# Optimization experiments

Hardware: AMD Instinct MI355X
Metric: run time of the kernel (lower is better)

The kernel has to match this reference:

```python
import jax, jax.numpy as jnp
import numpy as np

N_NODES = 50000
N_EDGES = 800000
IN_CH = 256
HID = 256
NUM_GRAPHS = 512
LEAKY_SLOPE = 0.01
EPS = 1e-5


def gcn_conv(x, src, dst, W, b):
    # src/dst already include self loops. Symmetric normalization D^-1/2 A_hat D^-1/2.
    deg = jnp.zeros((N_NODES,), x.dtype).at[dst].add(1.0)
    dinv = jax.lax.rsqrt(deg)  # deg >= 1 because of self loops
    norm = dinv[src] * dinv[dst]  # [E+N]
    h = x @ W  # [N, H] dense GEMM
    agg = jnp.zeros((N_NODES, W.shape[1]), x.dtype).at[dst].add(h[src] * norm[:, None])
    return agg + b


def layer_norm(x, w, b):
    mu = jnp.mean(x, axis=-1, keepdims=True)
    var = jnp.mean(jnp.square(x - mu), axis=-1, keepdims=True)
    return (x - mu) * jax.lax.rsqrt(var + EPS) * w + b


def setup_inputs() -> dict:
    key = jax.random.key(0)
    ks = jax.random.split(key, 8)
    x = jax.random.normal(ks[0], (N_NODES, IN_CH), dtype=jnp.float32)
    edge_index = jax.random.randint(ks[1], (2, N_EDGES), 0, N_NODES, dtype=jnp.int64)
    batch = jnp.sort(jax.random.randint(ks[2], (N_NODES,), 0, NUM_GRAPHS, dtype=jnp.int64))
    s1 = (2.0 / IN_CH) ** 0.5
    s2 = (2.0 / HID) ** 0.5
    W1 = jax.random.normal(ks[3], (IN_CH, HID), dtype=jnp.float32) * s1
    b1 = jnp.zeros((HID,), jnp.float32)
    W2 = jax.random.normal(ks[4], (HID, HID), dtype=jnp.float32) * s2
    b2 = jnp.zeros((HID,), jnp.float32)
    ln1_w = jnp.ones((HID,), jnp.float32)
    ln1_b = jnp.zeros((HID,), jnp.float32)
    ln2_w = jnp.ones((HID,), jnp.float32)
    ln2_b = jnp.zeros((HID,), jnp.float32)
    return {"x": x, "edge_index": edge_index, "batch": batch,
            "W1": W1, "b1": b1, "ln1_w": ln1_w, "ln1_b": ln1_b,
            "W2": W2, "b2": b2, "ln2_w": ln2_w, "ln2_b": ln2_b}


def reference(x, edge_index, batch, W1, b1, ln1_w, ln1_b, W2, b2, ln2_w, ln2_b):
    loop = jnp.arange(N_NODES, dtype=edge_index.dtype)
    src = jnp.concatenate([edge_index[0], loop])
    dst = jnp.concatenate([edge_index[1], loop])

    h = gcn_conv(x, src, dst, W1, b1)
    h = layer_norm(h, ln1_w, ln1_b)
    h = jnp.where(h >= 0, h, LEAKY_SLOPE * h)

    h = gcn_conv(h, src, dst, W2, b2)
    h = layer_norm(h, ln2_w, ln2_b)
    h = jnp.where(h >= 0, h, LEAKY_SLOPE * h)

    # global mean pool per graph (dropout is inference no-op)
    sums = jax.ops.segment_sum(h, batch, num_segments=NUM_GRAPHS)
    cnts = jax.ops.segment_sum(jnp.ones((N_NODES,), h.dtype), batch, num_segments=NUM_GRAPHS)
    return sums / jnp.maximum(cnts, 1.0)[:, None]
```

## Files before the change

### kernel.cpp

```cpp
#include <hip/hip_runtime.h>

#define N_NODES 50000
#define N_EDGES 800000
#define CH 256
#define NUM_GRAPHS 512
#define LEAKY 0.01f
#define LN_EPS 1e-5f
#define NBLK ((N_NODES + 255) / 256)

typedef __attribute__((ext_vector_type(4))) float f32x4;
typedef __attribute__((ext_vector_type(2))) float f32x2;
typedef __attribute__((ext_vector_type(8))) short bf16x8;

__device__ __forceinline__ float b2f(unsigned short u) {
    union { unsigned int i; float f; } x; x.i = ((unsigned int)u) << 16; return x.f;
}
__device__ __forceinline__ unsigned short f2b(float f) {
    union { float f; unsigned int i; } x; x.f = f;
    unsigned int r = x.i + 0x7fffu + ((x.i >> 16) & 1u);
    return (unsigned short)(r >> 16);
}
__device__ __forceinline__ f32x2 b2f2(unsigned int u) {
    union { unsigned int i; float f; } lo, hi;
    lo.i = u << 16; hi.i = u & 0xffff0000u;
    f32x2 r; r.x = lo.f; r.y = hi.f; return r;
}
__device__ __forceinline__ unsigned int pack2(float a, float b) {
    return (unsigned int)f2b(a) | ((unsigned int)f2b(b) << 16);
}

__global__ void zero_ints(int* __restrict__ p, int n) {
    int i = blockIdx.x * blockDim.x + threadIdx.x;
    if (i < n) p[i] = 0;
}

__global__ void count_deg(const int* __restrict__ dst, int* __restrict__ cnt) {
    int e = blockIdx.x * blockDim.x + threadIdx.x;
    if (e < N_EDGES) atomicAdd(&cnt[dst[e]], 1);
}

__global__ __launch_bounds__(256) void block_reduce(const int* __restrict__ cnt,
                                                    int* __restrict__ bsum,
                                                    float* __restrict__ dinv) {
    __shared__ int s[256];
    int tid = threadIdx.x;
    int i = blockIdx.x * 256 + tid;
    int v = (i < N_NODES) ? cnt[i] : 0;
    if (i < N_NODES) dinv[i] = rsqrtf(1.0f + (float)v);
    s[tid] = v;
    __syncthreads();
    #pragma unroll
    for (int off = 128; off > 0; off >>= 1) {
        if (tid < off) s[tid] += s[tid + off];
        __syncthreads();
    }
    if (tid == 0) bsum[blockIdx.x] = s[0];
}

__global__ __launch_bounds__(256) void scan_bsums(int* __restrict__ bsum) {
    __shared__ int s[256];
    int tid = threadIdx.x;
    int v = (tid < NBLK) ? bsum[tid] : 0;
    s[tid] = v;
    __syncthreads();
    #pragma unroll
    for (int off = 1; off < 256; off <<= 1) {
        int t = (tid >= off) ? s[tid - off] : 0;
        __syncthreads();
        s[tid] += t;
        __syncthreads();
    }
    if (tid < NBLK) bsum[tid] = s[tid] - v;
}

__global__ __launch_bounds__(256) void block_scan(const int* __restrict__ cnt,
                                                  const int* __restrict__ bsum,
                                                  int* __restrict__ rowptr,
                                                  int* __restrict__ cursor) {
    __shared__ int s[256];
    int tid = threadIdx.x;
    int i = blockIdx.x * 256 + tid;
    int v = (i < N_NODES) ? cnt[i] : 0;
    s[tid] = v;
    __syncthreads();
    #pragma unroll
    for (int off = 1; off < 256; off <<= 1) {
        int t = (tid >= off) ? s[tid - off] : 0;
        __syncthreads();
        s[tid] += t;
        __syncthreads();
    }
    if (i < N_NODES) {
        int val = bsum[blockIdx.x] + s[tid] - v;
        rowptr[i] = val;
        cursor[i] = val;
        if (i == N_NODES - 1) rowptr[N_NODES] = bsum[blockIdx.x] + s[tid];
    }
}

__global__ void fill_csr(const int* __restrict__ src, const int* __restrict__ dst,
                         int* __restrict__ cursor, int* __restrict__ col) {
    int e = blockIdx.x * blockDim.x + threadIdx.x;
    if (e < N_EDGES) {
        int d = dst[e];
        int p = atomicAdd(&cursor[d], 1);
        col[p] = src[e];
    }
}

__global__ void transpose_w(const float* __restrict__ W, unsigned short* __restrict__ WT) {
    int k = blockIdx.x;
    int n = threadIdx.x;
    WT[n * CH + k] = f2b(W[k * CH + n]);
}

#define BM 128
#define BN 128
#define BK 64
#define SWZ(row, kb) (((row) * 128 + (kb) * 16) ^ (((row) & 7) << 4))

__global__ __launch_bounds__(256) void gemm_bf16(const unsigned short* __restrict__ A,
                                                 const unsigned short* __restrict__ BT,
                                                 const float* __restrict__ dinv,
                                                 unsigned short* __restrict__ out) {
    __shared__ unsigned short As[BM * BK];
    __shared__ unsigned short Bs[BN * BK];
    const int row0 = blockIdx.x * BM;
    const int col0 = blockIdx.y * BN;
    const int tid = threadIdx.x;
    const int w = tid >> 6, l = tid & 63;
    const int wr = w >> 1, wc = w & 1;
    const int lr = l & 15, lg = l >> 4;

    f32x4 acc[4][4] = {};

    for (int k0 = 0; k0 < CH; k0 += BK) {
        #pragma unroll
        for (int it = 0; it < 4; it++) {
            int cidx = it * 256 + tid;
            int r = cidx >> 3, kb = cidx & 7;
            int grow = row0 + r;
            uint4 va = make_uint4(0u, 0u, 0u, 0u);
            if (grow < N_NODES) va = *(const uint4*)&A[(size_t)grow * CH + k0 + kb * 8];
            *(uint4*)((char*)As + SWZ(r, kb)) = va;
            uint4 vb = *(const uint4*)&BT[(size_t)(col0 + r) * CH + k0 + kb * 8];
            *(uint4*)((char*)Bs + SWZ(r, kb)) = vb;
        }
        __syncthreads();
        #pragma unroll
        for (int ks = 0; ks < 2; ks++) {
            bf16x8 af[4], bfr[4];
            #pragma unroll
            for (int fm = 0; fm < 4; fm++) {
                int r = wr * 64 + fm * 16 + lr;
                af[fm] = *(const bf16x8*)((const char*)As + SWZ(r, ks * 4 + lg));
            }
            #pragma unroll
            for (int fn = 0; fn < 4; fn++) {
                int r = wc * 64 + fn * 16 + lr;
                bfr[fn] = *(const bf16x8*)((const char*)Bs + SWZ(r, ks * 4 + lg));
            }
            #pragma unroll
            for (int fm = 0; fm < 4; fm++)
                #pragma unroll
                for (int fn = 0; fn < 4; fn++)
                    acc[fm][fn] = __builtin_amdgcn_mfma_f32_16x16x32_bf16(af[fm], bfr[fn], acc[fm][fn], 0, 0, 0);
        }
        __syncthreads();
    }
    #pragma unroll
    for (int fm = 0; fm < 4; fm++) {
        #pragma unroll
        for (int r = 0; r < 4; r++) {
            int grow = row0 + wr * 64 + fm * 16 + lg * 4 + r;
            if (grow < N_NODES) {
                float s = dinv[grow];
                #pragma unroll
                for (int fn = 0; fn < 4; fn++) {
                    int gcol = col0 + wc * 64 + fn * 16 + lr;
                    out[(size_t)grow * CH + gcol] = f2b(acc[fm][fn][r] * s);
                }
            }
        }
    }
}

__global__ __launch_bounds__(256) void gemm_f32a(const float* __restrict__ Af,
                                                 const unsigned short* __restrict__ BT,
                                                 const float* __restrict__ dinv,
                                                 unsigned short* __restrict__ out) {
    __shared__ unsigned short As[BM * BK];
    __shared__ unsigned short Bs[BN * BK];
    const int row0 = blockIdx.x * BM;
    const int col0 = blockIdx.y * BN;
    const int tid = threadIdx.x;
    const int w = tid >> 6, l = tid & 63;
    const int wr = w >> 1, wc = w & 1;
    const int lr = l & 15, lg = l >> 4;

    f32x4 acc[4][4] = {};

    for (int k0 = 0; k0 < CH; k0 += BK) {
        #pragma unroll
        for (int it = 0; it < 4; it++) {
            int cidx = it * 256 + tid;
            int r = cidx >> 3, kb = cidx & 7;
            int grow = row0 + r;
            uint4 ua = make_uint4(0u, 0u, 0u, 0u);
            if (grow < N_NODES) {
                const float* ap = &Af[(size_t)grow * CH + k0 + kb * 8];
                float4 v0 = *(const float4*)ap;
                float4 v1 = *(const float4*)(ap + 4);
                ua = make_uint4(pack2(v0.x, v0.y), pack2(v0.z, v0.w),
                                pack2(v1.x, v1.y), pack2(v1.z, v1.w));
            }
            *(uint4*)((char*)As + SWZ(r, kb)) = ua;
            uint4 vb = *(const uint4*)&BT[(size_t)(col0 + r) * CH + k0 + kb * 8];
            *(uint4*)((char*)Bs + SWZ(r, kb)) = vb;
        }
        __syncthreads();
        #pragma unroll
        for (int ks = 0; ks < 2; ks++) {
            bf16x8 af[4], bfr[4];
            #pragma unroll
            for (int fm = 0; fm < 4; fm++) {
                int r = wr * 64 + fm * 16 + lr;
                af[fm] = *(const bf16x8*)((const char*)As + SWZ(r, ks * 4 + lg));
            }
            #pragma unroll
            for (int fn = 0; fn < 4; fn++) {
                int r = wc * 64 + fn * 16 + lr;
                bfr[fn] = *(const bf16x8*)((const char*)Bs + SWZ(r, ks * 4 + lg));
            }
            #pragma unroll
            for (int fm = 0; fm < 4; fm++)
                #pragma unroll
                for (int fn = 0; fn < 4; fn++)
                    acc[fm][fn] = __builtin_amdgcn_mfma_f32_16x16x32_bf16(af[fm], bfr[fn], acc[fm][fn], 0, 0, 0);
        }
        __syncthreads();
    }
    #pragma unroll
    for (int fm = 0; fm < 4; fm++) {
        #pragma unroll
        for (int r = 0; r < 4; r++) {
            int grow = row0 + wr * 64 + fm * 16 + lg * 4 + r;
            if (grow < N_NODES) {
                float s = dinv[grow];
                #pragma unroll
                for (int fn = 0; fn < 4; fn++) {
                    int gcol = col0 + wc * 64 + fn * 16 + lr;
                    out[(size_t)grow * CH + gcol] = f2b(acc[fm][fn][r] * s);
                }
            }
        }
    }
}

__global__ __launch_bounds__(256) void agg_ln_bf16(const unsigned short* __restrict__ h,
                                                   const int* __restrict__ rowptr,
                                                   const int* __restrict__ col,
                                                   const float* __restrict__ dinv,
                                                   const float* __restrict__ bias,
                                                   const float* __restrict__ lnw,
                                                   const float* __restrict__ lnb,
                                                   unsigned short* __restrict__ out) {
    const int w = threadIdx.x >> 6, lane = threadIdx.x & 63;
    const int d = blockIdx.x * 4 + w;
    if (d >= N_NODES) return;
    const int c4 = lane * 4;
    const uint2* __restrict__ h2 = (const uint2*)h;

    f32x2 acc01, acc23;
    {
        uint2 u = h2[(unsigned)(d * 64 + lane)];
        acc01 = b2f2(u.x); acc23 = b2f2(u.y);
    }

    const int e0 = rowptr[d], e1 = rowptr[d + 1];
    for (int base = e0; base < e1; base += 64) {
        int nch = e1 - base; if (nch > 64) nch = 64;
        int cidx = (lane < nch) ? col[base + lane] : 0;
        int j = 0;
        for (; j + 8 <= nch; j += 8) {
            int s0 = __shfl(cidx, j),     s1 = __shfl(cidx, j + 1);
            int s2 = __shfl(cidx, j + 2), s3 = __shfl(cidx, j + 3);
            int s4 = __shfl(cidx, j + 4), s5 = __shfl(cidx, j + 5);
            int s6 = __shfl(cidx, j + 6), s7 = __shfl(cidx, j + 7);
            uint2 u0 = h2[(unsigned)(s0 * 64 + lane)];
            uint2 u1 = h2[(unsigned)(s1 * 64 + lane)];
            uint2 u2 = h2[(unsigned)(s2 * 64 + lane)];
            uint2 u3 = h2[(unsigned)(s3 * 64 + lane)];
            uint2 u4 = h2[(unsigned)(s4 * 64 + lane)];
            uint2 u5 = h2[(unsigned)(s5 * 64 + lane)];
            uint2 u6 = h2[(unsigned)(s6 * 64 + lane)];
            uint2 u7 = h2[(unsigned)(s7 * 64 + lane)];
            acc01 += b2f2(u0.x) + b2f2(u1.x) + b2f2(u2.x) + b2f2(u3.x);
            acc23 += b2f2(u0.y) + b2f2(u1.y) + b2f2(u2.y) + b2f2(u3.y);
            acc01 += b2f2(u4.x) + b2f2(u5.x) + b2f2(u6.x) + b2f2(u7.x);
            acc23 += b2f2(u4.y) + b2f2(u5.y) + b2f2(u6.y) + b2f2(u7.y);
        }
        for (; j + 4 <= nch; j += 4) {
            int s0 = __shfl(cidx, j),     s1 = __shfl(cidx, j + 1);
            int s2 = __shfl(cidx, j + 2), s3 = __shfl(cidx, j + 3);
            uint2 u0 = h2[(unsigned)(s0 * 64 + lane)];
            uint2 u1 = h2[(unsigned)(s1 * 64 + lane)];
            uint2 u2 = h2[(unsigned)(s2 * 64 + lane)];
            uint2 u3 = h2[(unsigned)(s3 * 64 + lane)];
            acc01 += b2f2(u0.x) + b2f2(u1.x) + b2f2(u2.x) + b2f2(u3.x);
            acc23 += b2f2(u0.y) + b2f2(u1.y) + b2f2(u2.y) + b2f2(u3.y);
        }
        for (; j < nch; j++) {
            int s = __shfl(cidx, j);
            uint2 u = h2[(unsigned)(s * 64 + lane)];
            acc01 += b2f2(u.x); acc23 += b2f2(u.y);
        }
    }
    float a0 = acc01.x, a1 = acc01.y, a2 = acc23.x, a3 = acc23.y;
    const float di = dinv[d];
    float4 bb = *(const float4*)&bias[c4];
    a0 = a0 * di + bb.x; a1 = a1 * di + bb.y; a2 = a2 * di + bb.z; a3 = a3 * di + bb.w;

    float s1 = a0 + a1 + a2 + a3;
    float s2 = a0 * a0 + a1 * a1 + a2 * a2 + a3 * a3;
    #pragma unroll
    for (int off = 32; off > 0; off >>= 1) {
        s1 += __shfl_xor(s1, off);
        s2 += __shfl_xor(s2, off);
    }
    const float mu = s1 * (1.0f / CH);
    const float rstd = rsqrtf(s2 * (1.0f / CH) - mu * mu + LN_EPS);
    float4 wv = *(const float4*)&lnw[c4];
    float4 bv = *(const float4*)&lnb[c4];
    float y0 = (a0 - mu) * rstd * wv.x + bv.x;
    float y1 = (a1 - mu) * rstd * wv.y + bv.y;
    float y2 = (a2 - mu) * rstd * wv.z + bv.z;
    float y3 = (a3 - mu) * rstd * wv.w + bv.w;
    y0 = (y0 >= 0.f) ? y0 : LEAKY * y0;
    y1 = (y1 >= 0.f) ? y1 : LEAKY * y1;
    y2 = (y2 >= 0.f) ? y2 : LEAKY * y2;
    y3 = (y3 >= 0.f) ? y3 : LEAKY * y3;
    *(ushort4*)&out[(size_t)d * CH + c4] = make_ushort4(f2b(y0), f2b(y1), f2b(y2), f2b(y3));
}

__global__ __launch_bounds__(256) void pool_mean_bf16(const unsigned short* __restrict__ feat,
                                                      const int* __restrict__ batch,
                                                      float* __restrict__ out) {
    const int g = blockIdx.x;
    const int w = threadIdx.x >> 6, lane = threadIdx.x & 63;
    int lo = 0, hi = N_NODES;
    while (lo < hi) { int mid = (lo + hi) >> 1; if (batch[mid] < g) lo = mid + 1; else hi = mid; }
    const int start = lo;
    hi = N_NODES;
    while (lo < hi) { int mid = (lo + hi) >> 1; if (batch[mid] < g + 1) lo = mid + 1; else hi = mid; }
    const int end = lo;

    float a0 = 0.f, a1 = 0.f, a2 = 0.f, a3 = 0.f;
    for (int n = start + w; n < end; n += 4) {
        ushort4 u = *(const ushort4*)&feat[(size_t)n * CH + lane * 4];
        a0 += b2f(u.x); a1 += b2f(u.y); a2 += b2f(u.z); a3 += b2f(u.w);
    }
    __shared__ float4 red[4][64];
    red[w][lane] = make_float4(a0, a1, a2, a3);
    __syncthreads();
    if (w == 0) {
        float4 t0 = red[0][lane], t1 = red[1][lane], t2 = red[2][lane], t3 = red[3][lane];
        const float inv = (end > start) ? 1.0f / (float)(end - start) : 0.0f;
        float4 o = make_float4((t0.x + t1.x + t2.x + t3.x) * inv,
                               (t0.y + t1.y + t2.y + t3.y) * inv,
                               (t0.z + t1.z + t2.z + t3.z) * inv,
                               (t0.w + t1.w + t2.w + t3.w) * inv);
        *(float4*)&out[(size_t)g * CH + lane * 4] = o;
    }
}

static inline size_t align256(size_t x) { return (x + 255) & ~(size_t)255; }

extern "C" void kernel_launch(void* const* d_in, const int* in_sizes, int n_in,
                              void* d_out, int out_size, void* d_ws, size_t ws_size,
                              hipStream_t stream) {
    const float* x    = (const float*)d_in[0];
    const int*   edge = (const int*)d_in[1];
    const int*   batch= (const int*)d_in[2];
    const float* W1   = (const float*)d_in[3];
    const float* b1   = (const float*)d_in[4];
    const float* ln1w = (const float*)d_in[5];
    const float* ln1b = (const float*)d_in[6];
    const float* W2   = (const float*)d_in[7];
    const float* b2   = (const float*)d_in[8];
    const float* ln2w = (const float*)d_in[9];
    const float* ln2b = (const float*)d_in[10];

    const int* src = edge;
    const int* dst = edge + N_EDGES;

    char* p = (char*)d_ws;
    int* cnt    = (int*)p;  p += align256(N_NODES * 4);
    int* cursor = (int*)p;  p += align256(N_NODES * 4);
    int* rowptr = (int*)p;  p += align256((N_NODES + 1) * 4);
    int* bsum   = (int*)p;  p += align256(NBLK * 4);
    float* dinv = (float*)p; p += align256(N_NODES * 4);
    int* col    = (int*)p;  p += align256(N_EDGES * 4);
    unsigned short* wt1 = (unsigned short*)p; p += align256(CH * CH * 2);
    unsigned short* wt2 = (unsigned short*)p; p += align256(CH * CH * 2);
    unsigned short* bufA = (unsigned short*)p; p += align256((size_t)N_NODES * CH * 2);
    unsigned short* bufB = (unsigned short*)p;

    zero_ints<<<(N_NODES + 255) / 256, 256, 0, stream>>>(cnt, N_NODES);
    count_deg<<<(N_EDGES + 255) / 256, 256, 0, stream>>>(dst, cnt);
    block_reduce<<<NBLK, 256, 0, stream>>>(cnt, bsum, dinv);
    scan_bsums<<<1, 256, 0, stream>>>(bsum);
    block_scan<<<NBLK, 256, 0, stream>>>(cnt, bsum, rowptr, cursor);
    fill_csr<<<(N_EDGES + 255) / 256, 256, 0, stream>>>(src, dst, cursor, col);

    transpose_w<<<CH, CH, 0, stream>>>(W1, wt1);
    transpose_w<<<CH, CH, 0, stream>>>(W2, wt2);

    dim3 ggrid((N_NODES + BM - 1) / BM, CH / BN);
    gemm_f32a<<<ggrid, 256, 0, stream>>>(x, wt1, dinv, bufA);
    agg_ln_bf16<<<(N_NODES + 3) / 4, 256, 0, stream>>>(bufA, rowptr, col, dinv, b1, ln1w, ln1b, bufB);
    gemm_bf16<<<ggrid, 256, 0, stream>>>(bufB, wt2, dinv, bufA);
    agg_ln_bf16<<<(N_NODES + 3) / 4, 256, 0, stream>>>(bufA, rowptr, col, dinv, b2, ln2w, ln2b, bufB);
    pool_mean_bf16<<<NUM_GRAPHS, 256, 0, stream>>>(bufB, batch, (float*)d_out);
}
```

Measured before the change: 303.2 us.

## Split aggregation into per-half-row gathers with separate LayerNorm pass

The fused gather+LayerNorm kernel is split so each wave gathers only half of a 256-channel row (128 channels, 4-byte loads), with blocks interleaved so both halves of the same nodes run close together. Partial sums and sums of squares go to a stats buffer, and a separate kernel (or the pooling kernel in layer 2) applies LayerNorm and LeakyReLU. The aim is to make each gathered row chunk smaller and raise parallelism for latency-bound random gathers. In exchange it adds an extra bf16 round trip for the pre-norm activations, an extra kernel launch, and twice the edge index reads and shuffles.

```diff
diff --git a/kernel.cpp b/kernel.cpp
--- a/kernel.cpp
+++ b/kernel.cpp
@@ -257,25 +257,23 @@
     }
 }
 
-__global__ __launch_bounds__(256) void agg_ln_bf16(const unsigned short* __restrict__ h,
+__global__ __launch_bounds__(256) void gather_half(const unsigned short* __restrict__ h,
                                                    const int* __restrict__ rowptr,
                                                    const int* __restrict__ col,
                                                    const float* __restrict__ dinv,
                                                    const float* __restrict__ bias,
-                                                   const float* __restrict__ lnw,
-                                                   const float* __restrict__ lnb,
-                                                   unsigned short* __restrict__ out) {
+                                                   unsigned short* __restrict__ raw,
+                                                   float* __restrict__ stats) {
     const int w = threadIdx.x >> 6, lane = threadIdx.x & 63;
-    const int d = blockIdx.x * 4 + w;
-    if (d >= N_NODES) return;
-    const int c4 = lane * 4;
-    const uint2* __restrict__ h2 = (const uint2*)h;
-
-    f32x2 acc01, acc23;
-    {
-        uint2 u = h2[(unsigned)(d * 64 + lane)];
-        acc01 = b2f2(u.x); acc23 = b2f2(u.y);
-    }
+    const unsigned b = blockIdx.x;
+    const int half  = (b >> 2) & 1;
+    const int group = (b >> 3) * 4 + (b & 3);
+    const int d = group * 4 + w;
+    const int doff = half * 64 + lane;
+    const uint* __restrict__ h1 = (const uint*)h;
+
+    f32x2 acc;
+    { uint u = h1[(size_t)d * 128 + doff]; acc = b2f2(u); }
 
     const int e0 = rowptr[d], e1 = rowptr[d + 1];
     for (int base = e0; base < e1; base += 64) {
@@ -287,55 +285,71 @@
             int s2 = __shfl(cidx, j + 2), s3 = __shfl(cidx, j + 3);
             int s4 = __shfl(cidx, j + 4), s5 = __shfl(cidx, j + 5);
             int s6 = __shfl(cidx, j + 6), s7 = __shfl(cidx, j + 7);
-            uint2 u0 = h2[(unsigned)(s0 * 64 + lane)];
-            uint2 u1 = h2[(unsigned)(s1 * 64 + lane)];
-            uint2 u2 = h2[(unsigned)(s2 * 64 + lane)];
-            uint2 u3 = h2[(unsigned)(s3 * 64 + lane)];
-            uint2 u4 = h2[(unsigned)(s4 * 64 + lane)];
-            uint2 u5 = h2[(unsigned)(s5 * 64 + lane)];
-            uint2 u6 = h2[(unsigned)(s6 * 64 + lane)];
-            uint2 u7 = h2[(unsigned)(s7 * 64 + lane)];
-            acc01 += b2f2(u0.x) + b2f2(u1.x) + b2f2(u2.x) + b2f2(u3.x);
-            acc23 += b2f2(u0.y) + b2f2(u1.y) + b2f2(u2.y) + b2f2(u3.y);
-            acc01 += b2f2(u4.x) + b2f2(u5.x) + b2f2(u6.x) + b2f2(u7.x);
-            acc23 += b2f2(u4.y) + b2f2(u5.y) + b2f2(u6.y) + b2f2(u7.y);
+            uint u0 = h1[(size_t)s0 * 128 + doff];
+            uint u1 = h1[(size_t)s1 * 128 + doff];
+            uint u2 = h1[(size_t)s2 * 128 + doff];
+            uint u3 = h1[(size_t)s3 * 128 + doff];
+            uint u4 = h1[(size_t)s4 * 128 + doff];
+            uint u5 = h1[(size_t)s5 * 128 + doff];
+            uint u6 = h1[(size_t)s6 * 128 + doff];
+            uint u7 = h1[(size_t)s7 * 128 + doff];
+            acc += b2f2(u0) + b2f2(u1) + b2f2(u2) + b2f2(u3);
+            acc += b2f2(u4) + b2f2(u5) + b2f2(u6) + b2f2(u7);
         }
         for (; j + 4 <= nch; j += 4) {
             int s0 = __shfl(cidx, j),     s1 = __shfl(cidx, j + 1);
             int s2 = __shfl(cidx, j + 2), s3 = __shfl(cidx, j + 3);
-            uint2 u0 = h2[(unsigned)(s0 * 64 + lane)];
-            uint2 u1 = h2[(unsigned)(s1 * 64 + lane)];
-            uint2 u2 = h2[(unsigned)(s2 * 64 + lane)];
-            uint2 u3 = h2[(unsigned)(s3 * 64 + lane)];
-            acc01 += b2f2(u0.x) + b2f2(u1.x) + b2f2(u2.x) + b2f2(u3.x);
-            acc23 += b2f2(u0.y) + b2f2(u1.y) + b2f2(u2.y) + b2f2(u3.y);
+            uint u0 = h1[(size_t)s0 * 128 + doff];
+            uint u1 = h1[(size_t)s1 * 128 + doff];
+            uint u2 = h1[(size_t)s2 * 128 + doff];
+            uint u3 = h1[(size_t)s3 * 128 + doff];
+            acc += b2f2(u0) + b2f2(u1) + b2f2(u2) + b2f2(u3);
         }
         for (; j < nch; j++) {
             int s = __shfl(cidx, j);
-            uint2 u = h2[(unsigned)(s * 64 + lane)];
-            acc01 += b2f2(u.x); acc23 += b2f2(u.y);
-        }
-    }
-    float a0 = acc01.x, a1 = acc01.y, a2 = acc23.x, a3 = acc23.y;
+            uint u = h1[(size_t)s * 128 + doff];
+            acc += b2f2(u);
+        }
+    }
     const float di = dinv[d];
-    float4 bb = *(const float4*)&bias[c4];
-    a0 = a0 * di + bb.x; a1 = a1 * di + bb.y; a2 = a2 * di + bb.z; a3 = a3 * di + bb.w;
-
-    float s1 = a0 + a1 + a2 + a3;
-    float s2 = a0 * a0 + a1 * a1 + a2 * a2 + a3 * a3;
+    const float2 bb = *(const float2*)&bias[doff * 2];
+    float a0 = acc.x * di + bb.x;
+    float a1 = acc.y * di + bb.y;
+
+    float s1 = a0 + a1;
+    float s2 = a0 * a0 + a1 * a1;
     #pragma unroll
     for (int off = 32; off > 0; off >>= 1) {
         s1 += __shfl_xor(s1, off);
         s2 += __shfl_xor(s2, off);
     }
-    const float mu = s1 * (1.0f / CH);
-    const float rstd = rsqrtf(s2 * (1.0f / CH) - mu * mu + LN_EPS);
+    if (lane == 0) {
+        stats[d * 4 + half * 2 + 0] = s1;
+        stats[d * 4 + half * 2 + 1] = s2;
+    }
+    ((uint*)raw)[(size_t)d * 128 + doff] = pack2(a0, a1);
+}
+
+__global__ __launch_bounds__(256) void ln_final(const unsigned short* __restrict__ raw,
+                                                const float* __restrict__ stats,
+                                                const float* __restrict__ lnw,
+                                                const float* __restrict__ lnb,
+                                                unsigned short* __restrict__ out) {
+    const int w = threadIdx.x >> 6, lane = threadIdx.x & 63;
+    const int d = blockIdx.x * 4 + w;
+    const int c4 = lane * 4;
+    uint2 u = ((const uint2*)raw)[(size_t)d * 64 + lane];
+    f32x2 a01 = b2f2(u.x), a23 = b2f2(u.y);
+    float4 st = *(const float4*)&stats[d * 4];
+    const float mu = (st.x + st.z) * (1.0f / CH);
+    const float var = (st.y + st.w) * (1.0f / CH) - mu * mu;
+    const float rstd = rsqrtf(var + LN_EPS);
     float4 wv = *(const float4*)&lnw[c4];
     float4 bv = *(const float4*)&lnb[c4];
-    float y0 = (a0 - mu) * rstd * wv.x + bv.x;
-    float y1 = (a1 - mu) * rstd * wv.y + bv.y;
-    float y2 = (a2 - mu) * rstd * wv.z + bv.z;
-    float y3 = (a3 - mu) * rstd * wv.w + bv.w;
+    float y0 = (a01.x - mu) * rstd * wv.x + bv.x;
+    float y1 = (a01.y - mu) * rstd * wv.y + bv.y;
+    float y2 = (a23.x - mu) * rstd * wv.z + bv.z;
+    float y3 = (a23.y - mu) * rstd * wv.w + bv.w;
     y0 = (y0 >= 0.f) ? y0 : LEAKY * y0;
     y1 = (y1 >= 0.f) ? y1 : LEAKY * y1;
     y2 = (y2 >= 0.f) ? y2 : LEAKY * y2;
@@ -343,11 +357,15 @@
     *(ushort4*)&out[(size_t)d * CH + c4] = make_ushort4(f2b(y0), f2b(y1), f2b(y2), f2b(y3));
 }
 
-__global__ __launch_bounds__(256) void pool_mean_bf16(const unsigned short* __restrict__ feat,
-                                                      const int* __restrict__ batch,
-                                                      float* __restrict__ out) {
+__global__ __launch_bounds__(256) void pool_ln(const unsigned short* __restrict__ raw,
+                                               const float* __restrict__ stats,
+                                               const float* __restrict__ lnw,
+                                               const float* __restrict__ lnb,
+                                               const int* __restrict__ batch,
+                                               float* __restrict__ out) {
     const int g = blockIdx.x;
     const int w = threadIdx.x >> 6, lane = threadIdx.x & 63;
+    const int c4 = lane * 4;
     int lo = 0, hi = N_NODES;
     while (lo < hi) { int mid = (lo + hi) >> 1; if (batch[mid] < g) lo = mid + 1; else hi = mid; }
     const int start = lo;
@@ -355,10 +373,24 @@
     while (lo < hi) { int mid = (lo + hi) >> 1; if (batch[mid] < g + 1) lo = mid + 1; else hi = mid; }
     const int end = lo;
 
+    float4 wv = *(const float4*)&lnw[c4];
+    float4 bv = *(const float4*)&lnb[c4];
     float a0 = 0.f, a1 = 0.f, a2 = 0.f, a3 = 0.f;
     for (int n = start + w; n < end; n += 4) {
-        ushort4 u = *(const ushort4*)&feat[(size_t)n * CH + lane * 4];
-        a0 += b2f(u.x); a1 += b2f(u.y); a2 += b2f(u.z); a3 += b2f(u.w);
+        uint2 u = ((const uint2*)raw)[(size_t)n * 64 + lane];
+        f32x2 r01 = b2f2(u.x), r23 = b2f2(u.y);
+        float4 st = *(const float4*)&stats[n * 4];
+        const float mu = (st.x + st.z) * (1.0f / CH);
+        const float var = (st.y + st.w) * (1.0f / CH) - mu * mu;
+        const float rstd = rsqrtf(var + LN_EPS);
+        float y0 = (r01.x - mu) * rstd * wv.x + bv.x;
+        float y1 = (r01.y - mu) * rstd * wv.y + bv.y;
+        float y2 = (r23.x - mu) * rstd * wv.z + bv.z;
+        float y3 = (r23.y - mu) * rstd * wv.w + bv.w;
+        a0 += (y0 >= 0.f) ? y0 : LEAKY * y0;
+        a1 += (y1 >= 0.f) ? y1 : LEAKY * y1;
+        a2 += (y2 >= 0.f) ? y2 : LEAKY * y2;
+        a3 += (y3 >= 0.f) ? y3 : LEAKY * y3;
     }
     __shared__ float4 red[4][64];
     red[w][lane] = make_float4(a0, a1, a2, a3);
@@ -400,11 +432,13 @@
     int* rowptr = (int*)p;  p += align256((N_NODES + 1) * 4);
     int* bsum   = (int*)p;  p += align256(NBLK * 4);
     float* dinv = (float*)p; p += align256(N_NODES * 4);
+    float* stats= (float*)p; p += align256((size_t)N_NODES * 4 * 4);
     int* col    = (int*)p;  p += align256(N_EDGES * 4);
     unsigned short* wt1 = (unsigned short*)p; p += align256(CH * CH * 2);
     unsigned short* wt2 = (unsigned short*)p; p += align256(CH * CH * 2);
     unsigned short* bufA = (unsigned short*)p; p += align256((size_t)N_NODES * CH * 2);
-    unsigned short* bufB = (unsigned short*)p;
+    unsigned short* bufB = (unsigned short*)p; p += align256((size_t)N_NODES * CH * 2);
+    unsigned short* bufC = (unsigned short*)p;
 
     zero_ints<<<(N_NODES + 255) / 256, 256, 0, stream>>>(cnt, N_NODES);
     count_deg<<<(N_EDGES + 255) / 256, 256, 0, stream>>>(dst, cnt);
@@ -417,9 +451,12 @@
     transpose_w<<<CH, CH, 0, stream>>>(W2, wt2);
 
     dim3 ggrid((N_NODES + BM - 1) / BM, CH / BN);
+    const int gblocks = (N_NODES / 4) * 2;
+
     gemm_f32a<<<ggrid, 256, 0, stream>>>(x, wt1, dinv, bufA);
-    agg_ln_bf16<<<(N_NODES + 3) / 4, 256, 0, stream>>>(bufA, rowptr, col, dinv, b1, ln1w, ln1b, bufB);
+    gather_half<<<gblocks, 256, 0, stream>>>(bufA, rowptr, col, dinv, b1, bufC, stats);
+    ln_final<<<N_NODES / 4, 256, 0, stream>>>(bufC, stats, ln1w, ln1b, bufB);
     gemm_bf16<<<ggrid, 256, 0, stream>>>(bufB, wt2, dinv, bufA);
-    agg_ln_bf16<<<(N_NODES + 3) / 4, 256, 0, stream>>>(bufA, rowptr, col, dinv, b2, ln2w, ln2b, bufB);
-    pool_mean_bf16<<<NUM_GRAPHS, 256, 0, stream>>>(bufB, batch, (float*)d_out);
-}
+    gather_half<<<gblocks, 256, 0, stream>>>(bufA, rowptr, col, dinv, b2, bufC, stats);
+    pool_ln<<<NUM_GRAPHS, 256, 0, stream>>>(bufC, stats, ln2w, ln2b, batch, (float*)d_out);
+}
```

Measured after the change: 315.0 us. +3.9%, slower.
